# Performance work log

Hardware: AMD Instinct MI355X
Metric: run time of the kernel (lower is better)

Reference implementation:

```python
import jax, jax.numpy as jnp
import numpy as np

T_STEPS = 64      # AR order p
MAX_T = 65536     # trajectory length
BATCH = 256       # number of sampled trajectories
STD = 0.3


def setup_inputs() -> dict:
    key = jax.random.key(0)
    k1, k2, k3 = jax.random.split(key, 3)
    raw = jax.random.normal(k1, (T_STEPS,), dtype=jnp.float32)
    # torch init: params / sum(|params|)
    params = raw / jnp.sum(jnp.abs(raw))
    bias = jax.random.uniform(k2, (1,), dtype=jnp.float32)
    noise = jax.random.normal(k3, (BATCH, MAX_T), dtype=jnp.float32)
    return {"params": params, "bias": bias, "noise": noise}


def _ar_means(params, bias, length):
    """AR(p) recurrence: mean_i = sum_k params[k] * x[i-1-k] + bias, x init = 0.
    State holds the last p values, most-recent-first (matches the reversed
    indexing inputs[i-1 : i-p-1 : -1] in the torch code)."""
    p = params.shape[0]

    def step(state, _):
        new = jnp.dot(state, params) + bias[0]
        state = jnp.concatenate([new[None], state[:-1]])
        return state, new

    init = jnp.zeros((p,), dtype=params.dtype)
    _, means = jax.lax.scan(step, init, None, length=length)
    return means  # [length]


def reference(params, bias, noise):
    # means of the Normal over the trajectory (deterministic, shared by batch)
    means = _ar_means(params, bias, noise.shape[1])  # [T]
    # reparameterized sample: actions = mean + std * eps, eps ~ N(0, 1)
    actions = means[None, :] + jnp.asarray(STD, noise.dtype) * noise  # [B, T]
    return actions
```

## Files before the change

kernel.cpp:

```cpp
#include <hip/hip_runtime.h>

#define T_LEN   65536
#define BATCH   256
#define P       64
#define K1_LEN  8192
#define K1_THREADS 256
#define DBLK    256

typedef float f4 __attribute__((ext_vector_type(4)));


__global__ __launch_bounds__(K1_THREADS, 1) void ar_k1(const float* __restrict__ params,
                                                       float* __restrict__ R) {
    __shared__ __align__(16) float Rl[K1_LEN];
    __shared__ float p[128];
    __shared__ float Wp[64][4];
    __shared__ __align__(16) float Vs[68];
    const int tid = threadIdx.x;
    if (tid < 128) p[tid] = (tid < P) ? params[tid] : 0.f;
    __syncthreads();

    if (tid < 64) {
        float z = 0.f;
        const float pk = p[tid];
        for (int t = 0; t < 64; ++t) {
            float y  = __shfl(z, 0) + 1.0f;
            float zn = __shfl_down(z, 1);
            if (tid == 63) zn = 0.f;
            z = fmaf(pk, y, zn);
            if (tid == 0) Rl[t] = y;
        }
    }
    __syncthreads();

    for (int L = 64; L <= K1_LEN; L <<= 1) {
        const bool last = (L == K1_LEN);
        {
            const int j = tid >> 2, c = tid & 3;
            const int mbase = c << 4;
            float w = 0.f;
            #pragma unroll
            for (int mm = 0; mm < 16; ++mm) {
                const int m = mbase + mm;
                w = fmaf(p[m + j], Rl[L - 1 - m], w);
            }
            Wp[j][c] = w;
        }
        __syncthreads();
        if (tid <= P) {
            const float wj  = (tid < P)
                ? (Wp[tid][0] + Wp[tid][1] + Wp[tid][2] + Wp[tid][3]) : 0.f;
            const float wm1 = (tid >= 1)
                ? (Wp[tid-1][0] + Wp[tid-1][1] + Wp[tid-1][2] + Wp[tid-1][3]) : 0.f;
            Vs[tid] = wj - wm1;
        }
        __syncthreads();
        if (tid < P) {
            const int tau = tid;
            float acc = Rl[tau];
            #pragma unroll
            for (int i = 0; i < P; ++i) {
                const int idx = (tau - i) > 0 ? (tau - i) : 0;
                const float v = (i <= tau) ? Vs[i] : 0.f;
                acc = fmaf(v, Rl[idx], acc);
            }
            if (last) R[L + tau] = acc; else Rl[L + tau] = acc;
        }
        {
            const f4* __restrict__ Rl4 = reinterpret_cast<const f4*>(Rl);
            f4* __restrict__ Rl4w = reinterpret_cast<f4*>(Rl);
            f4* __restrict__ Rg4  = reinterpret_cast<f4*>(R);
            const f4* __restrict__ V4 = reinterpret_cast<const f4*>(Vs);
            const int nq = (L - 64) >> 2;
            #pragma unroll 1
            for (int q = tid; q < nq; q += K1_THREADS) {
                f4 w4[17];
                #pragma unroll
                for (int j = 0; j < 17; ++j) w4[j] = Rl4[q + j];
                float a0 = w4[16].x, a1 = w4[16].y, a2 = w4[16].z, a3 = w4[16].w;
                #pragma unroll
                for (int g = 0; g < 16; ++g) {
                    const f4 v  = V4[g];
                    const f4 hi = w4[16 - g];
                    const f4 lo = w4[15 - g];
                    a0 = fmaf(v.x, hi.x, a0); a1 = fmaf(v.x, hi.y, a1);
                    a2 = fmaf(v.x, hi.z, a2); a3 = fmaf(v.x, hi.w, a3);
                    a0 = fmaf(v.y, lo.w, a0); a1 = fmaf(v.y, hi.x, a1);
                    a2 = fmaf(v.y, hi.y, a2); a3 = fmaf(v.y, hi.z, a3);
                    a0 = fmaf(v.z, lo.z, a0); a1 = fmaf(v.z, lo.w, a1);
                    a2 = fmaf(v.z, hi.x, a2); a3 = fmaf(v.z, hi.y, a3);
                    a0 = fmaf(v.w, lo.y, a0); a1 = fmaf(v.w, lo.z, a1);
                    a2 = fmaf(v.w, lo.w, a2); a3 = fmaf(v.w, hi.x, a3);
                }
                const float v64 = Vs[64];
                a0 = fmaf(v64, w4[0].x, a0); a1 = fmaf(v64, w4[0].y, a1);
                a2 = fmaf(v64, w4[0].z, a2); a3 = fmaf(v64, w4[0].w, a3);
                f4 o; o.x = a0; o.y = a1; o.z = a2; o.w = a3;
                if (last) Rg4[((L + 64) >> 2) + q] = o;
                else      Rl4w[((L + 64) >> 2) + q] = o;
            }
        }
        __syncthreads();
    }

    for (int j = tid; j < K1_LEN / 4; j += K1_THREADS)
        reinterpret_cast<f4*>(R)[j] = reinterpret_cast<const f4*>(Rl)[j];
}

__global__ __launch_bounds__(DBLK) void ar_double(const float* __restrict__ params,
                                                  float* __restrict__ R, const int L) {
    __shared__ float p[128];
    __shared__ float tl[P];
    __shared__ float Wp[64][4];
    __shared__ float V[P + 1];
    __shared__ float win[DBLK + P];
    const int tid = threadIdx.x;
    const int B0  = blockIdx.x * DBLK;
    if (tid < 128) p[tid] = (tid < P) ? params[tid] : 0.f;
    if (tid < P)   tl[tid] = R[L - 1 - tid];
    for (int j = tid; j < DBLK + P; j += DBLK) {
        const int g = B0 - P + j;
        win[j] = (g >= 0) ? R[g] : 0.f;
    }
    __syncthreads();
    {
        const int j = tid >> 2, c = tid & 3;
        const int mbase = c << 4;
        float w = 0.f;
        #pragma unroll
        for (int mm = 0; mm < 16; ++mm) {
            const int m = mbase + mm;
            w = fmaf(p[m + j], tl[m], w);
        }
        Wp[j][c] = w;
    }
    __syncthreads();
    if (tid <= P) {
        const float wj  = (tid < P)
            ? (Wp[tid][0] + Wp[tid][1] + Wp[tid][2] + Wp[tid][3]) : 0.f;
        const float wm1 = (tid >= 1)
            ? (Wp[tid-1][0] + Wp[tid-1][1] + Wp[tid-1][2] + Wp[tid-1][3]) : 0.f;
        V[tid] = wj - wm1;
    }
    __syncthreads();
    float acc = win[P + tid];
    #pragma unroll
    for (int i = 0; i <= P; ++i) acc = fmaf(V[i], win[P + tid - i], acc);
    R[L + B0 + tid] = acc;
}

__global__ __launch_bounds__(256) void ar_out(const float* __restrict__ R,
                                              const float* __restrict__ bias,
                                              const float* __restrict__ noise,
                                              float* __restrict__ out) {
    const int i4 = blockIdx.x * 256 + threadIdx.x;
    const float b = bias[0];
    const int t4 = i4 & (T_LEN / 4 - 1);
    const f4 r4 = reinterpret_cast<const f4*>(R)[t4];
    const f4 n4 = __builtin_nontemporal_load(reinterpret_cast<const f4*>(noise) + i4);
    f4 o;
    o.x = fmaf(0.3f, n4.x, b * r4.x);
    o.y = fmaf(0.3f, n4.y, b * r4.y);
    o.z = fmaf(0.3f, n4.z, b * r4.z);
    o.w = fmaf(0.3f, n4.w, b * r4.w);
    __builtin_nontemporal_store(o, reinterpret_cast<f4*>(out) + i4);
}

extern "C" void kernel_launch(void* const* d_in, const int* in_sizes, int n_in,
                              void* d_out, int out_size, void* d_ws, size_t ws_size,
                              hipStream_t stream) {
    const float* params = (const float*)d_in[0];
    const float* bias   = (const float*)d_in[1];
    const float* noise  = (const float*)d_in[2];
    float* out = (float*)d_out;
    float* R   = (float*)d_ws;

    hipLaunchKernelGGL(ar_k1, dim3(1), dim3(K1_THREADS), 0, stream, params, R);
    for (int L = 2 * K1_LEN; L < T_LEN; L <<= 1)
        hipLaunchKernelGGL(ar_double, dim3(L / DBLK), dim3(DBLK), 0, stream,
                           params, R, L);
    hipLaunchKernelGGL(ar_out, dim3((BATCH * (T_LEN / 4)) / 256), dim3(256),
                       0, stream, R, bias, noise, out);
}
```

Baseline: 168.0 us.

## Fuse final doubling stages into output kernel and compute doubling coefficients in k1

The single-block kernel now also computes the 65-tap doubling coefficient vectors for the last two doubling steps (16K→32K and 32K→64K) and stores them in the workspace. The separate ar_double launches are removed. The output kernel rebuilds its tile of the trajectory on the fly from the first 16K values using one or two 65-tap convolutions, then streams 8 batch rows per block. This cuts kernel launches and global round trips of R, at the cost of recomputing the convolution in each batch chunk (32 times per tile) and extra per-block latency before the noise stream starts.

```diff
diff --git a/kernel.cpp b/kernel.cpp
--- a/kernel.cpp
+++ b/kernel.cpp
@@ -5,7 +5,10 @@
 #define P       64
 #define K1_LEN  8192
 #define K1_THREADS 256
-#define DBLK    256
+#define W_TILE  1024
+#define BCHUNK  8
+#define VOFF    65536
+#define V3OFF   (VOFF + 80)
 
 typedef float f4 __attribute__((ext_vector_type(4)));
 
@@ -16,6 +19,8 @@
     __shared__ float p[128];
     __shared__ float Wp[64][4];
     __shared__ __align__(16) float Vs[68];
+    __shared__ __align__(16) float tailb[192];
+    __shared__ float t3[128];
     const int tid = threadIdx.x;
     if (tid < 128) p[tid] = (tid < P) ? params[tid] : 0.f;
     __syncthreads();
@@ -96,41 +101,24 @@
                 a0 = fmaf(v64, w4[0].x, a0); a1 = fmaf(v64, w4[0].y, a1);
                 a2 = fmaf(v64, w4[0].z, a2); a3 = fmaf(v64, w4[0].w, a3);
                 f4 o; o.x = a0; o.y = a1; o.z = a2; o.w = a3;
-                if (last) Rg4[((L + 64) >> 2) + q] = o;
-                else      Rl4w[((L + 64) >> 2) + q] = o;
-            }
-        }
-        __syncthreads();
-    }
-
-    for (int j = tid; j < K1_LEN / 4; j += K1_THREADS)
-        reinterpret_cast<f4*>(R)[j] = reinterpret_cast<const f4*>(Rl)[j];
-}
-
-__global__ __launch_bounds__(DBLK) void ar_double(const float* __restrict__ params,
-                                                  float* __restrict__ R, const int L) {
-    __shared__ float p[128];
-    __shared__ float tl[P];
-    __shared__ float Wp[64][4];
-    __shared__ float V[P + 1];
-    __shared__ float win[DBLK + P];
-    const int tid = threadIdx.x;
-    const int B0  = blockIdx.x * DBLK;
-    if (tid < 128) p[tid] = (tid < P) ? params[tid] : 0.f;
-    if (tid < P)   tl[tid] = R[L - 1 - tid];
-    for (int j = tid; j < DBLK + P; j += DBLK) {
-        const int g = B0 - P + j;
-        win[j] = (g >= 0) ? R[g] : 0.f;
-    }
-    __syncthreads();
+                if (last) {
+                    Rg4[((L + 64) >> 2) + q] = o;
+                    if (q >= 1984) reinterpret_cast<f4*>(tailb)[q - 1984] = o;
+                } else {
+                    Rl4w[((L + 64) >> 2) + q] = o;
+                }
+            }
+        }
+        __syncthreads();
+    }
+
     {
-        const int j = tid >> 2, c = tid & 3;
-        const int mbase = c << 4;
+        const int j = tid >> 2, c = tid & 3, mbase = c << 4;
         float w = 0.f;
         #pragma unroll
         for (int mm = 0; mm < 16; ++mm) {
             const int m = mbase + mm;
-            w = fmaf(p[m + j], tl[m], w);
+            w = fmaf(p[m + j], tailb[191 - m], w);
         }
         Wp[j][c] = w;
     }
@@ -140,30 +128,133 @@
             ? (Wp[tid][0] + Wp[tid][1] + Wp[tid][2] + Wp[tid][3]) : 0.f;
         const float wm1 = (tid >= 1)
             ? (Wp[tid-1][0] + Wp[tid-1][1] + Wp[tid-1][2] + Wp[tid-1][3]) : 0.f;
-        V[tid] = wj - wm1;
-    }
-    __syncthreads();
-    float acc = win[P + tid];
+        const float v = wj - wm1;
+        Vs[tid] = v;
+        R[VOFF + tid] = v;
+    }
+    __syncthreads();
+    if (tid < 128) {
+        float acc = tailb[64 + tid];
+        #pragma unroll
+        for (int i = 0; i <= P; ++i)
+            acc = fmaf(Vs[i], tailb[64 + tid - i], acc);
+        t3[tid] = acc;
+    }
+    __syncthreads();
+    {
+        const int j = tid >> 2, c = tid & 3, mbase = c << 4;
+        float w = 0.f;
+        #pragma unroll
+        for (int mm = 0; mm < 16; ++mm) {
+            const int m = mbase + mm;
+            w = fmaf(p[m + j], t3[127 - m], w);
+        }
+        Wp[j][c] = w;
+    }
+    __syncthreads();
+    if (tid <= P) {
+        const float wj  = (tid < P)
+            ? (Wp[tid][0] + Wp[tid][1] + Wp[tid][2] + Wp[tid][3]) : 0.f;
+        const float wm1 = (tid >= 1)
+            ? (Wp[tid-1][0] + Wp[tid-1][1] + Wp[tid-1][2] + Wp[tid-1][3]) : 0.f;
+        R[V3OFF + tid] = wj - wm1;
+    }
+
+    for (int j = tid; j < K1_LEN / 4; j += K1_THREADS)
+        reinterpret_cast<f4*>(R)[j] = reinterpret_cast<const f4*>(Rl)[j];
+}
+
+__global__ __launch_bounds__(256) void ar_out_fused(const float* __restrict__ R,
+                                                    const float* __restrict__ bias,
+                                                    const float* __restrict__ noise,
+                                                    float* __restrict__ out) {
+    __shared__ __align__(16) float Rt[W_TILE];
+    __shared__ float winA[W_TILE + 64];
+    __shared__ float winB[W_TILE + 128];
+    __shared__ float V2l[72], V3l[72];
+    const int tid  = threadIdx.x;
+    const int tile = blockIdx.x & 63;
+    const int bc   = blockIdx.x >> 6;
+    const int t0   = tile * W_TILE;
+    const float b  = bias[0];
+
+    if (tid < 65)       V2l[tid] = R[VOFF + tid];
+    else if (tid < 130) V3l[tid - 65] = R[V3OFF + (tid - 65)];
+
+    f4 rt;
+    if (t0 < 16384) {
+        const f4 r = reinterpret_cast<const f4*>(R)[(t0 >> 2) + tid];
+        rt.x = b * r.x; rt.y = b * r.y; rt.z = b * r.z; rt.w = b * r.w;
+    } else if (t0 < 32768) {
+        const int u0 = t0 - 16384;
+        for (int k = tid; k < W_TILE + 64; k += 256) {
+            const int u = u0 - 64 + k;
+            winA[k] = (u >= 0) ? R[u] : 0.f;
+        }
+        __syncthreads();
+        for (int j = tid; j < W_TILE; j += 256) {
+            float acc = winA[64 + j];
+            #pragma unroll
+            for (int i = 0; i <= P; ++i)
+                acc = fmaf(V2l[i], winA[64 + j - i], acc);
+            Rt[j] = b * acc;
+        }
+        __syncthreads();
+        rt = reinterpret_cast<const f4*>(Rt)[tid];
+    } else {
+        const int tau0 = t0 - 32768;
+        const int s0   = tau0 - 64;
+        if (tau0 >= 16384) {
+            const int wb0 = s0 - 16448;
+            for (int k = tid; k < W_TILE + 128; k += 256) {
+                const int u = wb0 + k;
+                winB[k] = (u >= 0) ? R[u] : 0.f;
+            }
+        }
+        __syncthreads();
+        for (int k = tid; k < W_TILE + 64; k += 256) {
+            const int u = s0 + k;
+            float v;
+            if (u < 0) {
+                v = 0.f;
+            } else if (u < 16384) {
+                v = R[u];
+            } else {
+                float a = winB[k + 64];
+                #pragma unroll
+                for (int i = 0; i <= P; ++i)
+                    a = fmaf(V2l[i], winB[k + 64 - i], a);
+                v = a;
+            }
+            winA[k] = v;
+        }
+        __syncthreads();
+        for (int j = tid; j < W_TILE; j += 256) {
+            float acc = winA[64 + j];
+            #pragma unroll
+            for (int i = 0; i <= P; ++i)
+                acc = fmaf(V3l[i], winA[64 + j - i], acc);
+            Rt[j] = b * acc;
+        }
+        __syncthreads();
+        rt = reinterpret_cast<const f4*>(Rt)[tid];
+    }
+
+    const int nb4 = T_LEN >> 2;
+    const int col = (t0 >> 2) + tid;
+    const f4* __restrict__ n4 = reinterpret_cast<const f4*>(noise);
+    f4* __restrict__ o4 = reinterpret_cast<f4*>(out);
     #pragma unroll
-    for (int i = 0; i <= P; ++i) acc = fmaf(V[i], win[P + tid - i], acc);
-    R[L + B0 + tid] = acc;
-}
-
-__global__ __launch_bounds__(256) void ar_out(const float* __restrict__ R,
-                                              const float* __restrict__ bias,
-                                              const float* __restrict__ noise,
-                                              float* __restrict__ out) {
-    const int i4 = blockIdx.x * 256 + threadIdx.x;
-    const float b = bias[0];
-    const int t4 = i4 & (T_LEN / 4 - 1);
-    const f4 r4 = reinterpret_cast<const f4*>(R)[t4];
-    const f4 n4 = __builtin_nontemporal_load(reinterpret_cast<const f4*>(noise) + i4);
-    f4 o;
-    o.x = fmaf(0.3f, n4.x, b * r4.x);
-    o.y = fmaf(0.3f, n4.y, b * r4.y);
-    o.z = fmaf(0.3f, n4.z, b * r4.z);
-    o.w = fmaf(0.3f, n4.w, b * r4.w);
-    __builtin_nontemporal_store(o, reinterpret_cast<f4*>(out) + i4);
+    for (int bi = 0; bi < BCHUNK; ++bi) {
+        const int idx = (bc * BCHUNK + bi) * nb4 + col;
+        const f4 n = __builtin_nontemporal_load(n4 + idx);
+        f4 o;
+        o.x = fmaf(0.3f, n.x, rt.x);
+        o.y = fmaf(0.3f, n.y, rt.y);
+        o.z = fmaf(0.3f, n.z, rt.z);
+        o.w = fmaf(0.3f, n.w, rt.w);
+        __builtin_nontemporal_store(o, o4 + idx);
+    }
 }
 
 extern "C" void kernel_launch(void* const* d_in, const int* in_sizes, int n_in,
@@ -176,9 +267,6 @@
     float* R   = (float*)d_ws;
 
     hipLaunchKernelGGL(ar_k1, dim3(1), dim3(K1_THREADS), 0, stream, params, R);
-    for (int L = 2 * K1_LEN; L < T_LEN; L <<= 1)
-        hipLaunchKernelGGL(ar_double, dim3(L / DBLK), dim3(DBLK), 0, stream,
-                           params, R, L);
-    hipLaunchKernelGGL(ar_out, dim3((BATCH * (T_LEN / 4)) / 256), dim3(256),
-                       0, stream, R, bias, noise, out);
+    hipLaunchKernelGGL(ar_out_fused, dim3(64 * 32), dim3(256), 0, stream,
+                       R, bias, noise, out);
 }
```

After: 168.7 us. No clear change (+0.4%).
